# Optimization experiments

Measured on AMD Instinct MI355X. Metric: run time of the kernel, lower is better.

The kernel has to match this reference:

```python
import jax, jax.numpy as jnp
import numpy as np
from jax import lax

G = 4            # split_groups = ceil(256*9 / 576)
CIN_G = 64       # input channels per CiM array group
ABITS = 4
Q_LEVELS = 2 ** ABITS - 1
Q_WIDTH = 4.0    # qrelu clipping width (merged psum range)
Q_OFFSET = 0.0
BN_EPS = 1e-5


def ste_sign(x):
    # signed binarizer: {-1, +1}
    return jnp.where(x >= 0, 1.0, -1.0).astype(x.dtype)


def ste_round(x):
    return jnp.round(x)


def setup_inputs() -> dict:
    key = jax.random.key(0)
    k0, k1 = jax.random.split(key)
    x = jax.random.normal(k0, (32, 256, 32, 32), dtype=jnp.float32)
    weight = jax.random.normal(k1, (256, 256, 3, 3), dtype=jnp.float32) * 0.05
    gamma = jnp.ones((1024,), dtype=jnp.float32)
    beta = jnp.zeros((1024,), dtype=jnp.float32)
    return {"x": x, "weight": weight, "gamma": gamma, "beta": beta}


def _forward(x, weight, gamma, beta):
    B, Cin, H, W = x.shape
    Cout = weight.shape[0]
    # --- binarize weights (per-output-channel |w| mean scaling) ---
    alpha = jnp.mean(jnp.abs(weight), axis=(1, 2, 3), keepdims=True)  # [Cout,1,1,1]
    w_bin = ste_sign(weight) * alpha
    # --- split input channels into G CiM groups; each group emits its own partial sum ---
    # grouped conv: weights [G*Cout, Cin/G, 3, 3]; group g output uses input chans g*CIN_G:(g+1)*CIN_G
    w_g = jnp.concatenate([w_bin[:, g * CIN_G:(g + 1) * CIN_G] for g in range(G)], axis=0)
    psum = lax.conv_general_dilated(
        x, w_g, window_strides=(1, 1), padding="SAME",
        feature_group_count=G,
        dimension_numbers=("NCHW", "OIHW", "NCHW"))  # [B, G*Cout, H, W]
    # --- BatchNorm2d over G*Cout channels (training-mode batch stats) ---
    mean = jnp.mean(psum, axis=(0, 2, 3))
    var = jnp.var(psum, axis=(0, 2, 3))
    inv = lax.rsqrt(var + BN_EPS) * gamma
    y = psum * inv[None, :, None, None] + (beta - mean * inv)[None, :, None, None]
    # --- hardtanh + signed binarize ---
    y = jnp.clip(y, -1.0, 1.0)
    y = ste_sign(y)
    # --- merge: sum the G partial-sum groups back to Cout channels ---
    y = y.reshape(B, G, Cout, H, W).sum(axis=1)  # values in [-G, G]
    # --- qrelu: abits-level uniform quantized ReLU on [offset, offset+width] ---
    u = jnp.clip((y - Q_OFFSET) / Q_WIDTH, 0.0, 1.0)
    q = ste_round(u * Q_LEVELS) / Q_LEVELS * Q_WIDTH + Q_OFFSET
    return q


def reference(x, weight, gamma, beta):
    return _forward(x, weight, gamma, beta)
```

## Files before the change

### kernel.cpp

```cpp
#include <hip/hip_runtime.h>

#define OFF_PSUM   0UL
#define OFF_ALPHA  134217728UL
#define OFF_INV    134218752UL
#define OFF_BT     134222848UL

__global__ __launch_bounds__(256) void k_alpha(const float* __restrict__ w,
                                               float* __restrict__ alpha) {
#pragma clang fp contract(off)
    __shared__ float buf[2304];
    int co = blockIdx.x, t = threadIdx.x;
    const float* p = w + (size_t)co * 2304;
    for (int i = t; i < 2304; i += 256) buf[i] = p[i];
    __syncthreads();
    if (t == 0) {
        float s = 0.f;
#pragma unroll 16
        for (int k = 0; k < 2304; ++k) s = s + fabsf(buf[k]);
        alpha[co] = s / 2304.0f;
    }
}

__global__ __launch_bounds__(256) void k_wsaT(const float* __restrict__ w,
                                              const float* __restrict__ alpha,
                                              float* __restrict__ wsaT) {
    int item = blockIdx.x * 256 + threadIdx.x;
    int co = item & 255;
    int rest = item >> 8;
    int ci = rest & 63;
    int t9 = rest >> 6;
    int tap = t9 % 9, g = t9 / 9;
    float av = alpha[co];
    float wv = w[((size_t)co * 256 + g * 64 + ci) * 9 + tap];
    wsaT[item] = (wv >= 0.f) ? av : -av;
}

__global__ __launch_bounds__(512, 4) void k_conv(const float* __restrict__ x,
                                                 const float* __restrict__ wsaT,
                                                 float* __restrict__ psum) {
#pragma clang fp contract(off)
    __shared__ float xs[6][34][68];
    int bx = blockIdx.x;
    int band = bx & 7, g = (bx >> 3) & 3, b = bx >> 5;
    int t = threadIdx.x;

    const float* xg = x + (size_t)(b * 256 + g * 64) * 1024;
#pragma unroll 1
    for (int i = 0; i < 26; ++i) {
        int idx = i * 512 + t;
        if (idx < 13056) {
            int ci = idx & 63, col = (idx >> 6) % 34, row = idx / 2176;
            int gr = band * 4 + row - 1, gc = col - 1;
            float v = (gr >= 0 && gr < 32 && gc >= 0 && gc < 32)
                        ? xg[(size_t)ci * 1024 + gr * 32 + gc] : 0.f;
            xs[row][col][ci] = v;
        }
    }
    __syncthreads();

    int wid = t >> 6, lane = t & 63;
    int r = lane >> 5, m = lane & 31;
    int h0 = band * 4 + r;
    int cobase = __builtin_amdgcn_readfirstlane(wid * 32);

    float acc0[32], acc1[32];
#pragma unroll
    for (int j = 0; j < 32; ++j) { acc0[j] = 0.f; acc1[j] = 0.f; }

#pragma unroll 1
    for (int kh = 0; kh < 3; ++kh)
#pragma unroll 1
        for (int kw = 0; kw < 3; ++kw) {
            int tap = kh * 3 + kw;
            const float* bp0 = &xs[r + kh][m + kw][0];
            const float* bp1 = &xs[r + 2 + kh][m + kw][0];
            const float* wt = wsaT + (((size_t)(g * 9 + tap) * 64) << 8) + cobase;
#pragma unroll
            for (int c = 0; c < 4; ++c) {
                float xv0[16], xv1[16];
#pragma unroll
                for (int q = 0; q < 4; ++q) {
                    float4 a = *(const float4*)(bp0 + c * 16 + q * 4);
                    xv0[q * 4 + 0] = a.x; xv0[q * 4 + 1] = a.y;
                    xv0[q * 4 + 2] = a.z; xv0[q * 4 + 3] = a.w;
                    float4 d = *(const float4*)(bp1 + c * 16 + q * 4);
                    xv1[q * 4 + 0] = d.x; xv1[q * 4 + 1] = d.y;
                    xv1[q * 4 + 2] = d.z; xv1[q * 4 + 3] = d.w;
                }
#pragma unroll
                for (int ci = 0; ci < 16; ++ci) {
                    const float* wr = wt + ((c * 16 + ci) << 8);
#pragma unroll
                    for (int j = 0; j < 32; ++j)
                        acc0[j] = fmaf(xv0[ci], wr[j], acc0[j]);
#pragma unroll
                    for (int j = 0; j < 32; ++j)
                        acc1[j] = fmaf(xv1[ci], wr[j], acc1[j]);
                }
            }
        }

#pragma unroll
    for (int j = 0; j < 32; ++j) {
        int co = cobase + j;
        size_t rowo = ((size_t)b * 1024 + g * 256 + co) * 32;
        psum[(rowo + h0) * 32 + m]     = acc0[j];
        psum[(rowo + h0 + 2) * 32 + m] = acc1[j];
    }
}

__device__ __forceinline__ float chain_sum_1024(const float* pb, float s) {
#pragma clang fp contract(off)
    float4 A[16], B[16];
#pragma unroll
    for (int u = 0; u < 16; ++u) A[u] = *(const float4*)(pb + u * 4);
#pragma unroll 1
    for (int g = 0; g < 8; ++g) {
        const float* p1 = pb + (2 * g + 1) * 64;
#pragma unroll
        for (int u = 0; u < 16; ++u) B[u] = *(const float4*)(p1 + u * 4);
#pragma unroll
        for (int u = 0; u < 16; ++u) {
            s = s + A[u].x; s = s + A[u].y; s = s + A[u].z; s = s + A[u].w;
        }
        const float* p2 = pb + (2 * g + 2) * 64;
        if (g < 7) {
#pragma unroll
            for (int u = 0; u < 16; ++u) A[u] = *(const float4*)(p2 + u * 4);
        }
#pragma unroll
        for (int u = 0; u < 16; ++u) {
            s = s + B[u].x; s = s + B[u].y; s = s + B[u].z; s = s + B[u].w;
        }
    }
    return s;
}

__global__ __launch_bounds__(64, 1) void k_stats(const float* __restrict__ psum,
                                                 const float* __restrict__ gamma,
                                                 const float* __restrict__ beta,
                                                 float* __restrict__ invA,
                                                 float* __restrict__ btA) {
#pragma clang fp contract(off)
    __shared__ float buf[2][1024];
    __shared__ float res[1];
    int ch = blockIdx.x, t = threadIdx.x;
    const float* base = psum + (size_t)ch * 1024;

    float4 pre[4];
#pragma unroll
    for (int r = 0; r < 4; ++r) pre[r] = *(const float4*)(base + r * 256 + t * 4);
#pragma unroll
    for (int r = 0; r < 4; ++r) *(float4*)&buf[0][r * 256 + t * 4] = pre[r];
    __syncthreads();

    float s = 0.f;
    for (int b = 0; b < 32; ++b) {
        if (b + 1 < 32) {
            const float* nb = base + (size_t)(b + 1) * 1048576;
#pragma unroll
            for (int r = 0; r < 4; ++r) pre[r] = *(const float4*)(nb + r * 256 + t * 4);
        }
        if (t == 0) s = chain_sum_1024(buf[b & 1], s);
        __syncthreads();
        if (b + 1 < 32) {
#pragma unroll
            for (int r = 0; r < 4; ++r) *(float4*)&buf[(b + 1) & 1][r * 256 + t * 4] = pre[r];
        }
        __syncthreads();
    }
    if (t == 0) res[0] = s / 32768.0f;
    __syncthreads();
    float mean = res[0];

#pragma unroll
    for (int r = 0; r < 4; ++r) pre[r] = *(const float4*)(base + r * 256 + t * 4);
    {
        float4 sq[4];
#pragma unroll
        for (int r = 0; r < 4; ++r) {
            float d0 = pre[r].x - mean; sq[r].x = d0 * d0;
            float d1 = pre[r].y - mean; sq[r].y = d1 * d1;
            float d2 = pre[r].z - mean; sq[r].z = d2 * d2;
            float d3 = pre[r].w - mean; sq[r].w = d3 * d3;
        }
#pragma unroll
        for (int r = 0; r < 4; ++r) *(float4*)&buf[0][r * 256 + t * 4] = sq[r];
    }
    __syncthreads();

    float v = 0.f;
    for (int b = 0; b < 32; ++b) {
        if (b + 1 < 32) {
            const float* nb = base + (size_t)(b + 1) * 1048576;
#pragma unroll
            for (int r = 0; r < 4; ++r) pre[r] = *(const float4*)(nb + r * 256 + t * 4);
        }
        if (t == 0) v = chain_sum_1024(buf[b & 1], v);
        __syncthreads();
        if (b + 1 < 32) {
            float4 sq[4];
#pragma unroll
            for (int r = 0; r < 4; ++r) {
                float d0 = pre[r].x - mean; sq[r].x = d0 * d0;
                float d1 = pre[r].y - mean; sq[r].y = d1 * d1;
                float d2 = pre[r].z - mean; sq[r].z = d2 * d2;
                float d3 = pre[r].w - mean; sq[r].w = d3 * d3;
            }
#pragma unroll
            for (int r = 0; r < 4; ++r) *(float4*)&buf[(b + 1) & 1][r * 256 + t * 4] = sq[r];
        }
        __syncthreads();
    }
    if (t == 0) {
        float var = v / 32768.0f;
        float sq = sqrtf(var + 1e-5f);
        float inv = 1.0f / sq;
        inv = inv * gamma[ch];
        float mb = mean * inv;
        invA[ch] = inv;
        btA[ch] = beta[ch] - mb;
    }
}

__global__ __launch_bounds__(256) void k_apply(const float* __restrict__ psum,
                                               const float* __restrict__ invA,
                                               const float* __restrict__ btA,
                                               float* __restrict__ out) {
#pragma clang fp contract(off)
    int idx = blockIdx.x * 256 + threadIdx.x;
    int w4 = (idx & 7) * 4;
    int hh = (idx >> 3) & 31;
    int co = (idx >> 8) & 255;
    int b  = idx >> 16;

    float s0 = 0.f, s1 = 0.f, s2 = 0.f, s3 = 0.f;
    for (int g = 0; g < 4; ++g) {
        int ch = g * 256 + co;
        const float4 p = *(const float4*)(psum + (((size_t)b * 1024 + ch) * 32 + hh) * 32 + w4);
        float iv = invA[ch], bt = btA[ch];
        float y0 = p.x * iv; y0 = y0 + bt;
        float y1 = p.y * iv; y1 = y1 + bt;
        float y2 = p.z * iv; y2 = y2 + bt;
        float y3 = p.w * iv; y3 = y3 + bt;
        s0 = s0 + ((y0 >= 0.f) ? 1.f : -1.f);
        s1 = s1 + ((y1 >= 0.f) ? 1.f : -1.f);
        s2 = s2 + ((y2 >= 0.f) ? 1.f : -1.f);
        s3 = s3 + ((y3 >= 0.f) ? 1.f : -1.f);
    }
    float4 q;
    {
        float u, rr, qq;
        u = s0 * 0.25f; u = fminf(fmaxf(u, 0.f), 1.f); rr = rintf(u * 15.f); qq = rr / 15.f; q.x = qq * 4.f;
        u = s1 * 0.25f; u = fminf(fmaxf(u, 0.f), 1.f); rr = rintf(u * 15.f); qq = rr / 15.f; q.y = qq * 4.f;
        u = s2 * 0.25f; u = fminf(fmaxf(u, 0.f), 1.f); rr = rintf(u * 15.f); qq = rr / 15.f; q.z = qq * 4.f;
        u = s3 * 0.25f; u = fminf(fmaxf(u, 0.f), 1.f); rr = rintf(u * 15.f); qq = rr / 15.f; q.w = qq * 4.f;
    }
    *(float4*)(out + (((size_t)b * 256 + co) * 32 + hh) * 32 + w4) = q;
}

extern "C" void kernel_launch(void* const* d_in, const int* in_sizes, int n_in,
                              void* d_out, int out_size, void* d_ws, size_t ws_size,
                              hipStream_t stream) {
    (void)in_sizes; (void)n_in; (void)out_size; (void)ws_size;
    const float* x     = (const float*)d_in[0];
    const float* w     = (const float*)d_in[1];
    const float* gamma = (const float*)d_in[2];
    const float* beta  = (const float*)d_in[3];
    float* out = (float*)d_out;
    char* ws = (char*)d_ws;
    float* psum  = (float*)(ws + OFF_PSUM);
    float* alpha = (float*)(ws + OFF_ALPHA);
    float* invA  = (float*)(ws + OFF_INV);
    float* btA   = (float*)(ws + OFF_BT);
    float* wsaT  = out;

    hipLaunchKernelGGL(k_alpha, dim3(256),  dim3(256), 0, stream, w, alpha);
    hipLaunchKernelGGL(k_wsaT,  dim3(2304), dim3(256), 0, stream, w, alpha, wsaT);
    hipLaunchKernelGGL(k_conv,  dim3(1024), dim3(512), 0, stream, x, wsaT, psum);
    hipLaunchKernelGGL(k_stats, dim3(1024), dim3(64),  0, stream, psum, gamma, beta, invA, btA);
    hipLaunchKernelGGL(k_apply, dim3(8192), dim3(256), 0, stream, psum, invA, btA, out);
}
```

Measured before the change: 905.5 us.

## Compute BN channel stats with one thread per channel instead of one block

The statistics kernel now gives each thread one channel. Each thread keeps its own serial summation chain for the mean and then for the variance, in the same order as before, reading psum straight from global memory into four rotating register buffers. This removes the staging through shared memory and the two barriers per batch image, along with the idle 63 threads per block in the old scheme. The cost is that the whole kernel runs as only 16 wavefronts on 16 CUs, so it relies on each lane issuing enough in-flight loads. It also uses a large per-thread register footprint for the prefetch buffers.

```diff
diff --git a/kernel.cpp b/kernel.cpp
--- a/kernel.cpp
+++ b/kernel.cpp
@@ -109,118 +109,80 @@
     }
 }
 
-__device__ __forceinline__ float chain_sum_1024(const float* pb, float s) {
-#pragma clang fp contract(off)
-    float4 A[16], B[16];
-#pragma unroll
-    for (int u = 0; u < 16; ++u) A[u] = *(const float4*)(pb + u * 4);
-#pragma unroll 1
-    for (int g = 0; g < 8; ++g) {
-        const float* p1 = pb + (2 * g + 1) * 64;
-#pragma unroll
-        for (int u = 0; u < 16; ++u) B[u] = *(const float4*)(p1 + u * 4);
-#pragma unroll
-        for (int u = 0; u < 16; ++u) {
-            s = s + A[u].x; s = s + A[u].y; s = s + A[u].z; s = s + A[u].w;
-        }
-        const float* p2 = pb + (2 * g + 2) * 64;
-        if (g < 7) {
-#pragma unroll
-            for (int u = 0; u < 16; ++u) A[u] = *(const float4*)(p2 + u * 4);
-        }
-#pragma unroll
-        for (int u = 0; u < 16; ++u) {
-            s = s + B[u].x; s = s + B[u].y; s = s + B[u].z; s = s + B[u].w;
-        }
-    }
-    return s;
-}
-
 __global__ __launch_bounds__(64, 1) void k_stats(const float* __restrict__ psum,
                                                  const float* __restrict__ gamma,
                                                  const float* __restrict__ beta,
                                                  float* __restrict__ invA,
                                                  float* __restrict__ btA) {
 #pragma clang fp contract(off)
-    __shared__ float buf[2][1024];
-    __shared__ float res[1];
-    int ch = blockIdx.x, t = threadIdx.x;
-    const float* base = psum + (size_t)ch * 1024;
-
-    float4 pre[4];
-#pragma unroll
-    for (int r = 0; r < 4; ++r) pre[r] = *(const float4*)(base + r * 256 + t * 4);
-#pragma unroll
-    for (int r = 0; r < 4; ++r) *(float4*)&buf[0][r * 256 + t * 4] = pre[r];
-    __syncthreads();
+    int ch = blockIdx.x * 64 + threadIdx.x;
+    const float* lb = psum + (size_t)ch * 1024;
+
+#define LOADG(BUF, GI)                                                           \
+    do { int _g = (GI);                                                          \
+        const float* _p = lb + ((size_t)(_g >> 4) * 1048576) + ((_g & 15) * 64); \
+        _Pragma("unroll")                                                        \
+        for (int u = 0; u < 16; ++u) BUF[u] = *(const float4*)(_p + u * 4);      \
+    } while (0)
+
+#define ADDG(BUF)                                                                \
+    do { _Pragma("unroll")                                                       \
+        for (int u = 0; u < 16; ++u) {                                           \
+            s = s + BUF[u].x; s = s + BUF[u].y;                                  \
+            s = s + BUF[u].z; s = s + BUF[u].w; }                                \
+    } while (0)
+
+#define ADDVG(BUF)                                                               \
+    do { _Pragma("unroll")                                                       \
+        for (int u = 0; u < 16; ++u) {                                           \
+            float d0 = BUF[u].x - mean; float q0 = d0 * d0; v = v + q0;          \
+            float d1 = BUF[u].y - mean; float q1 = d1 * d1; v = v + q1;          \
+            float d2 = BUF[u].z - mean; float q2 = d2 * d2; v = v + q2;          \
+            float d3 = BUF[u].w - mean; float q3 = d3 * d3; v = v + q3; }        \
+    } while (0)
+
+    float4 P[16], Q[16], R[16], T[16];
 
     float s = 0.f;
-    for (int b = 0; b < 32; ++b) {
-        if (b + 1 < 32) {
-            const float* nb = base + (size_t)(b + 1) * 1048576;
-#pragma unroll
-            for (int r = 0; r < 4; ++r) pre[r] = *(const float4*)(nb + r * 256 + t * 4);
-        }
-        if (t == 0) s = chain_sum_1024(buf[b & 1], s);
-        __syncthreads();
-        if (b + 1 < 32) {
-#pragma unroll
-            for (int r = 0; r < 4; ++r) *(float4*)&buf[(b + 1) & 1][r * 256 + t * 4] = pre[r];
-        }
-        __syncthreads();
-    }
-    if (t == 0) res[0] = s / 32768.0f;
-    __syncthreads();
-    float mean = res[0];
-
-#pragma unroll
-    for (int r = 0; r < 4; ++r) pre[r] = *(const float4*)(base + r * 256 + t * 4);
-    {
-        float4 sq[4];
-#pragma unroll
-        for (int r = 0; r < 4; ++r) {
-            float d0 = pre[r].x - mean; sq[r].x = d0 * d0;
-            float d1 = pre[r].y - mean; sq[r].y = d1 * d1;
-            float d2 = pre[r].z - mean; sq[r].z = d2 * d2;
-            float d3 = pre[r].w - mean; sq[r].w = d3 * d3;
-        }
-#pragma unroll
-        for (int r = 0; r < 4; ++r) *(float4*)&buf[0][r * 256 + t * 4] = sq[r];
-    }
-    __syncthreads();
+    LOADG(P, 0); LOADG(Q, 1); LOADG(R, 2);
+#pragma unroll 1
+    for (int g = 0; g < 512; g += 4) {
+        LOADG(T, g + 3);
+        ADDG(P);
+        if (g + 4 < 512) { LOADG(P, g + 4); }
+        ADDG(Q);
+        if (g + 5 < 512) { LOADG(Q, g + 5); }
+        ADDG(R);
+        if (g + 6 < 512) { LOADG(R, g + 6); }
+        ADDG(T);
+    }
+    float mean = s / 32768.0f;
 
     float v = 0.f;
-    for (int b = 0; b < 32; ++b) {
-        if (b + 1 < 32) {
-            const float* nb = base + (size_t)(b + 1) * 1048576;
-#pragma unroll
-            for (int r = 0; r < 4; ++r) pre[r] = *(const float4*)(nb + r * 256 + t * 4);
-        }
-        if (t == 0) v = chain_sum_1024(buf[b & 1], v);
-        __syncthreads();
-        if (b + 1 < 32) {
-            float4 sq[4];
-#pragma unroll
-            for (int r = 0; r < 4; ++r) {
-                float d0 = pre[r].x - mean; sq[r].x = d0 * d0;
-                float d1 = pre[r].y - mean; sq[r].y = d1 * d1;
-                float d2 = pre[r].z - mean; sq[r].z = d2 * d2;
-                float d3 = pre[r].w - mean; sq[r].w = d3 * d3;
-            }
-#pragma unroll
-            for (int r = 0; r < 4; ++r) *(float4*)&buf[(b + 1) & 1][r * 256 + t * 4] = sq[r];
-        }
-        __syncthreads();
-    }
-    if (t == 0) {
-        float var = v / 32768.0f;
-        float sq = sqrtf(var + 1e-5f);
-        float inv = 1.0f / sq;
-        inv = inv * gamma[ch];
-        float mb = mean * inv;
-        invA[ch] = inv;
-        btA[ch] = beta[ch] - mb;
-    }
+    LOADG(P, 0); LOADG(Q, 1); LOADG(R, 2);
+#pragma unroll 1
+    for (int g = 0; g < 512; g += 4) {
+        LOADG(T, g + 3);
+        ADDVG(P);
+        if (g + 4 < 512) { LOADG(P, g + 4); }
+        ADDVG(Q);
+        if (g + 5 < 512) { LOADG(Q, g + 5); }
+        ADDVG(R);
+        if (g + 6 < 512) { LOADG(R, g + 6); }
+        ADDVG(T);
+    }
+
+    float var = v / 32768.0f;
+    float sq = sqrtf(var + 1e-5f);
+    float inv = 1.0f / sq;
+    inv = inv * gamma[ch];
+    float mb = mean * inv;
+    invA[ch] = inv;
+    btA[ch] = beta[ch] - mb;
+
+#undef LOADG
+#undef ADDG
+#undef ADDVG
 }
 
 __global__ __launch_bounds__(256) void k_apply(const float* __restrict__ psum,
@@ -278,6 +240,6 @@
     hipLaunchKernelGGL(k_alpha, dim3(256),  dim3(256), 0, stream, w, alpha);
     hipLaunchKernelGGL(k_wsaT,  dim3(2304), dim3(256), 0, stream, w, alpha, wsaT);
     hipLaunchKernelGGL(k_conv,  dim3(1024), dim3(512), 0, stream, x, wsaT, psum);
-    hipLaunchKernelGGL(k_stats, dim3(1024), dim3(64),  0, stream, psum, gamma, beta, invA, btA);
+    hipLaunchKernelGGL(k_stats, dim3(16),   dim3(64),  0, stream, psum, gamma, beta, invA, btA);
     hipLaunchKernelGGL(k_apply, dim3(8192), dim3(256), 0, stream, psum, invA, btA, out);
 }
```

New measurement: 1.343 ms. +48.3%, slower.
